# Optimization experiments

Measured on AMD Instinct MI355X. Metric: run time of the kernel, lower is better.

Reference implementation:

```python
import jax, jax.numpy as jnp
import numpy as np

B, T, D = 8, 4096, 768
H, HD, K = 12, 64, 32
TAU, THRESH = 12.5, 0.5
A_PARAM, B_PARAM, DT = 0.7, 0.8, 1.0  # nn.Parameters read via .item() -> scalar constants
N_FHN_STEPS = 2


def setup_inputs() -> dict:
    key = jax.random.key(0)
    k0, k1, k2, k3 = jax.random.split(key, 4)
    x = jax.random.normal(k0, (B, T, D), jnp.float32)
    spectral_basis = jax.random.normal(k1, (B, T, K), jnp.float32)
    w_qkv = jax.random.normal(k2, (3 * D, D), jnp.float32) * 0.02
    w_out = jax.random.normal(k3, (D, D), jnp.float32) * 0.02
    spectral_filter = jnp.ones((H, 32), jnp.float32) * 0.5
    return {"x": x, "spectral_basis": spectral_basis, "w_qkv": w_qkv,
            "w_out": w_out, "spectral_filter": spectral_filter}


def _fhn(stim):
    # Original expands stim [b,h,k] -> [b,h,k,head_dim] (constant along d), runs FHN,
    # then means over d. Values are identical along d, so amax over d == |stim| and the
    # mean is the identity; the math collapses exactly to per-element dynamics on [b,h,k].
    scale = jnp.maximum(jnp.abs(stim), 1e-6)          # == abs().amax(-1).clamp(1e-6)
    stim_normed = stim / scale
    gate = jax.nn.sigmoid((jnp.abs(stim) - THRESH) * 10.0)
    I = stim_normed * (0.1 + 0.9 * gate)
    alpha = DT / TAU
    denom = 1.0 + alpha * B_PARAM
    v = jnp.zeros_like(stim)
    w = jnp.zeros_like(stim)
    for _ in range(N_FHN_STEPS):  # fixed small n_steps, unrolled
        dv = v - (v * v * v) / 3.0 - w + I
        v_next = v + dv * DT
        w_next = (w + (v_next + A_PARAM) * alpha) / denom
        v = jnp.clip(v_next, -3.0, 3.0)
        w = jnp.clip(w_next, -3.0, 3.0)
    return v * scale


def reference(x, spectral_basis, w_qkv, w_out, spectral_filter):
    Bs, Ts, Ds = x.shape
    k = spectral_basis.shape[-1]
    qkv = x @ w_qkv.T                                   # [B,T,3D]
    qkv = qkv.reshape(Bs, Ts, 3, H, HD).transpose(2, 0, 3, 1, 4)  # three,b,h,t,d
    q, kk, v = qkv[0], qkv[1], qkv[2]
    q_spec = jnp.einsum('bhtd,btk->bhkd', q, spectral_basis)
    k_spec = jnp.einsum('bhtd,btk->bhkd', kk, spectral_basis)
    attn_spec = jnp.einsum('bhkd,bhkd->bhk', q_spec, k_spec) / (HD ** 0.5)
    filt = jax.nn.sigmoid(spectral_filter[:, :k])       # [H,k]
    attn_spec = attn_spec * filt[None, :, :]
    fhn_response = _fhn(attn_spec)                      # [B,H,k]
    v_spec = jnp.einsum('bhtd,btk->bhkd', v, spectral_basis)
    out_spec = fhn_response[..., None] * v_spec         # [B,H,k,d]
    out = jnp.einsum('bhkd,btk->bhtd', out_spec, spectral_basis)
    out = out.transpose(0, 2, 1, 3).reshape(Bs, Ts, Ds)  # b t (h d)
    return out @ w_out.T
```

## Files before the change

### kernel.cpp

```cpp
#include <hip/hip_runtime.h>

#define Bc 8
#define Tc 4096
#define Dc 768
#define Hc 12
#define HDc 64
#define Kc 32
#define TD3 2304
#define WQKV_F (TD3 * Dc)
#define WALL_F ((TD3 + Dc) * Dc)
#define SB_F (Bc * Tc * Kc)
#define XS_F (Bc * Kc * Dc)

typedef __attribute__((ext_vector_type(8))) short short8;
typedef __attribute__((ext_vector_type(4))) short short4v;
typedef __attribute__((ext_vector_type(4))) float float4v;

__device__ __forceinline__ float bf2f(unsigned short u) {
    unsigned v = ((unsigned)u) << 16;
    return __builtin_bit_cast(float, v);
}
__device__ __forceinline__ unsigned short f2bf(float f) {
    unsigned u = __builtin_bit_cast(unsigned, f);
    u += 0x7FFFu + ((u >> 16) & 1u);
    return (unsigned short)(u >> 16);
}

__device__ __forceinline__ void split8(const float* p, short8& hi, short8& lo) {
#pragma unroll
    for (int i = 0; i < 8; ++i) {
        unsigned short h = f2bf(p[i]);
        hi[i] = (short)h;
        lo[i] = (short)f2bf(p[i] - bf2f(h));
    }
}
__device__ __forceinline__ void split4(const float4v v, short4v& h, short4v& l) {
#pragma unroll
    for (int q = 0; q < 4; ++q) {
        unsigned short hb = f2bf(v[q]);
        h[q] = (short)hb;
        l[q] = (short)f2bf(v[q] - bf2f(hb));
    }
}

__global__ __launch_bounds__(256) void kconv(const float* __restrict__ wqkv,
                                             const float* __restrict__ wout,
                                             const float* __restrict__ sb,
                                             short* __restrict__ w_hi, short* __restrict__ w_lo,
                                             short* __restrict__ sb_hi, short* __restrict__ sb_lo,
                                             short* __restrict__ sbT_hi, short* __restrict__ sbT_lo) {
    int i = (blockIdx.x * 256 + threadIdx.x) * 4;
    if (i < WALL_F) {
        const float* src = (i < WQKV_F) ? (wqkv + i) : (wout + (i - WQKV_F));
        float4v v = *(const float4v*)src;
        short4v h, l;
        split4(v, h, l);
        *(short4v*)(w_hi + i) = h;
        *(short4v*)(w_lo + i) = l;
    } else {
        int j = i - WALL_F;
        float4v v = *(const float4v*)(sb + j);
        short4v h, l;
        split4(v, h, l);
        *(short4v*)(sb_hi + j) = h;
        *(short4v*)(sb_lo + j) = l;
        int b   = j >> 17;
        int rem = j & (Tc * Kc - 1);
        int t = rem >> 5, k = rem & 31;
        size_t tb = (size_t)b * Kc * Tc;
#pragma unroll
        for (int q = 0; q < 4; ++q) {
            sbT_hi[tb + (size_t)(k + q) * Tc + t] = h[q];
            sbT_lo[tb + (size_t)(k + q) * Tc + t] = l[q];
        }
    }
}

__global__ __launch_bounds__(256) void k1_xspec(const float* __restrict__ x,
                                                const short* __restrict__ sbT_hi,
                                                const short* __restrict__ sbT_lo,
                                                float* __restrict__ pb) {
    int tid  = threadIdx.x;
    int w    = tid >> 6;
    int lane = tid & 63;
    int col  = lane & 15;
    int quad = lane >> 4;

    int bid = blockIdx.x;
    int b  = bid >> 6;
    int dt = (bid >> 4) & 3;
    int tc = bid & 15;
    int d0 = dt * 192;
    size_t bT = (size_t)b * Tc + (size_t)tc * 256;

    float4v acc[2][3];
#pragma unroll
    for (int mi = 0; mi < 2; ++mi)
#pragma unroll
        for (int ni = 0; ni < 3; ++ni) acc[mi][ni] = (float4v){0.f, 0.f, 0.f, 0.f};

#pragma unroll 2
    for (int ks = 0; ks < 8; ++ks) {
        int t8 = tc * 256 + ks * 32 + quad * 8;
        short8 ah[2], al[2];
#pragma unroll
        for (int mi = 0; mi < 2; ++mi) {
            size_t ai = ((size_t)b * Kc + mi * 16 + col) * Tc + t8;
            ah[mi] = *(const short8*)(sbT_hi + ai);
            al[mi] = *(const short8*)(sbT_lo + ai);
        }
#pragma unroll
        for (int ni = 0; ni < 3; ++ni) {
            int nc = d0 + (w * 3 + ni) * 16 + col;
            float bv[8];
#pragma unroll
            for (int j = 0; j < 8; ++j)
                bv[j] = x[(bT + ks * 32 + quad * 8 + j) * Dc + nc];
            short8 bh, bl;
            split8(bv, bh, bl);
#pragma unroll
            for (int mi = 0; mi < 2; ++mi) {
                acc[mi][ni] = __builtin_amdgcn_mfma_f32_16x16x32_bf16(ah[mi], bh, acc[mi][ni], 0, 0, 0);
                acc[mi][ni] = __builtin_amdgcn_mfma_f32_16x16x32_bf16(al[mi], bh, acc[mi][ni], 0, 0, 0);
                acc[mi][ni] = __builtin_amdgcn_mfma_f32_16x16x32_bf16(ah[mi], bl, acc[mi][ni], 0, 0, 0);
            }
        }
    }

    float* pbp = pb + (size_t)tc * XS_F;
#pragma unroll
    for (int mi = 0; mi < 2; ++mi)
#pragma unroll
        for (int ni = 0; ni < 3; ++ni)
#pragma unroll
            for (int r = 0; r < 4; ++r) {
                int kk = mi * 16 + quad * 4 + r;
                int dd = d0 + (w * 3 + ni) * 16 + col;
                pbp[((size_t)(b * Kc + kk)) * Dc + dd] = acc[mi][ni][r];
            }
}

__global__ __launch_bounds__(256) void k1r_reduce(const float* __restrict__ pb,
                                                  short* __restrict__ xs_hi,
                                                  short* __restrict__ xs_lo) {
    int i = (blockIdx.x * 256 + threadIdx.x) * 4;
    float4v s = (float4v){0.f, 0.f, 0.f, 0.f};
#pragma unroll
    for (int p = 0; p < 16; ++p) {
        float4v v = *(const float4v*)(pb + (size_t)p * XS_F + i);
#pragma unroll
        for (int q = 0; q < 4; ++q) s[q] += v[q];
    }
    short4v h, l;
    split4(s, h, l);
    *(short4v*)(xs_hi + i) = h;
    *(short4v*)(xs_lo + i) = l;
}

__global__ __launch_bounds__(256) void k2_qkv(const short* __restrict__ xs_hi,
                                              const short* __restrict__ xs_lo,
                                              const short* __restrict__ w_hi,
                                              const short* __restrict__ w_lo,
                                              float* __restrict__ c1) {
    int lane = threadIdx.x & 63;
    int w    = threadIdx.x >> 6;
    int m    = lane & 15, quad = lane >> 4;
    int mb = blockIdx.x & 7;
    int nb = blockIdx.x >> 3;
    int m0 = mb * 32;
    int n0 = nb * 64 + w * 16;

    const short* a0h = xs_hi + (size_t)(m0 + m) * Dc + quad * 8;
    const short* a0l = xs_lo + (size_t)(m0 + m) * Dc + quad * 8;
    const short* a1h = a0h + (size_t)16 * Dc;
    const short* a1l = a0l + (size_t)16 * Dc;
    const short* bhp = w_hi + (size_t)(n0 + m) * Dc + quad * 8;
    const short* blp = w_lo + (size_t)(n0 + m) * Dc + quad * 8;

    float4v acc0 = (float4v){0.f, 0.f, 0.f, 0.f};
    float4v acc1 = (float4v){0.f, 0.f, 0.f, 0.f};
#pragma unroll 4
    for (int s = 0; s < 24; ++s) {
        short8 bh = *(const short8*)(bhp + s * 32);
        short8 bl = *(const short8*)(blp + s * 32);
        short8 h0 = *(const short8*)(a0h + s * 32);
        short8 l0 = *(const short8*)(a0l + s * 32);
        short8 h1 = *(const short8*)(a1h + s * 32);
        short8 l1 = *(const short8*)(a1l + s * 32);
        acc0 = __builtin_amdgcn_mfma_f32_16x16x32_bf16(h0, bh, acc0, 0, 0, 0);
        acc0 = __builtin_amdgcn_mfma_f32_16x16x32_bf16(l0, bh, acc0, 0, 0, 0);
        acc0 = __builtin_amdgcn_mfma_f32_16x16x32_bf16(h0, bl, acc0, 0, 0, 0);
        acc1 = __builtin_amdgcn_mfma_f32_16x16x32_bf16(h1, bh, acc1, 0, 0, 0);
        acc1 = __builtin_amdgcn_mfma_f32_16x16x32_bf16(l1, bh, acc1, 0, 0, 0);
        acc1 = __builtin_amdgcn_mfma_f32_16x16x32_bf16(h1, bl, acc1, 0, 0, 0);
    }
    float* cp0 = c1 + (size_t)(m0 + quad * 4) * TD3 + n0 + m;
    float* cp1 = cp0 + (size_t)16 * TD3;
#pragma unroll
    for (int r = 0; r < 4; ++r) {
        cp0[(size_t)r * TD3] = acc0[r];
        cp1[(size_t)r * TD3] = acc1[r];
    }
}

__global__ __launch_bounds__(64) void k3_fhn(const float* __restrict__ c1,
                                             const float* __restrict__ sfilt,
                                             short* __restrict__ av_hi,
                                             short* __restrict__ av_lo) {
    int idx = blockIdx.x * 64 + threadIdx.x;
    int kk = idx & 31;
    int bh = idx >> 5;
    int h  = bh % Hc;
    int r  = (bh / Hc) * Kc + kk;

    const float* qp = c1 + (size_t)r * TD3 + h * HDc;
    const float* kp = qp + Dc;
    float s = 0.f;
#pragma unroll
    for (int dd = 0; dd < HDc; ++dd) s = fmaf(qp[dd], kp[dd], s);
    s *= 0.125f;

    float filt = 1.f / (1.f + __expf(-sfilt[h * 32 + kk]));
    s *= filt;

    float as    = fabsf(s);
    float scale = fmaxf(as, 1e-6f);
    float sn    = s / scale;
    float gate  = 1.f / (1.f + __expf(-(as - 0.5f) * 10.f));
    float I     = sn * (0.1f + 0.9f * gate);
    const float alpha = 0.08f;
    const float denom = 1.064f;
    float v = 0.f, w = 0.f;
#pragma unroll
    for (int it = 0; it < 2; ++it) {
        float dv = v - (v * v * v) / 3.f - w + I;
        float vn = v + dv;
        float wn = (w + (vn + 0.7f) * alpha) / denom;
        v = fminf(fmaxf(vn, -3.f), 3.f);
        w = fminf(fmaxf(wn, -3.f), 3.f);
    }
    float fv = v * scale;

    const float* vp = c1 + (size_t)r * TD3 + 2 * Dc + h * HDc;
    short* ohp = av_hi + (size_t)r * Dc + h * HDc;
    short* olp = av_lo + (size_t)r * Dc + h * HDc;
#pragma unroll
    for (int i = 0; i < 16; ++i) {
        float4v vv = *(const float4v*)(vp + i * 4);
#pragma unroll
        for (int q = 0; q < 4; ++q) vv[q] *= fv;
        short4v hv, lv;
        split4(vv, hv, lv);
        *(short4v*)(ohp + i * 4) = hv;
        *(short4v*)(olp + i * 4) = lv;
    }
}

__global__ __launch_bounds__(256) void k4_proj(const short* __restrict__ av_hi,
                                               const short* __restrict__ av_lo,
                                               const short* __restrict__ wo_hi,
                                               const short* __restrict__ wo_lo,
                                               short* __restrict__ pT_hi,
                                               short* __restrict__ pT_lo) {
    int wave = blockIdx.x * 4 + (threadIdx.x >> 6);
    int lane = threadIdx.x & 63;
    int mb = wave & 15;
    int nt = wave >> 4;
    int m0 = mb * 16, n0 = nt * 16;
    int m = lane & 15, quad = lane >> 4;

    const short* ahp = av_hi + (size_t)(m0 + m) * Dc + quad * 8;
    const short* alp = av_lo + (size_t)(m0 + m) * Dc + quad * 8;
    const short* bhp = wo_hi + (size_t)(n0 + m) * Dc + quad * 8;
    const short* blp = wo_lo + (size_t)(n0 + m) * Dc + quad * 8;

    float4v acc = (float4v){0.f, 0.f, 0.f, 0.f};
#pragma unroll 4
    for (int s = 0; s < 24; ++s) {
        short8 ah = *(const short8*)(ahp + s * 32);
        short8 al = *(const short8*)(alp + s * 32);
        short8 bh = *(const short8*)(bhp + s * 32);
        short8 bl = *(const short8*)(blp + s * 32);
        acc = __builtin_amdgcn_mfma_f32_16x16x32_bf16(ah, bh, acc, 0, 0, 0);
        acc = __builtin_amdgcn_mfma_f32_16x16x32_bf16(al, bh, acc, 0, 0, 0);
        acc = __builtin_amdgcn_mfma_f32_16x16x32_bf16(ah, bl, acc, 0, 0, 0);
    }
    short4v hv, lv;
    split4(acc, hv, lv);
    size_t o = (size_t)(n0 + m) * (Bc * Kc) + m0 + quad * 4;
    *(short4v*)(pT_hi + o) = hv;
    *(short4v*)(pT_lo + o) = lv;
}

__global__ __launch_bounds__(256) void k5_out(const short* __restrict__ pT_hi,
                                              const short* __restrict__ pT_lo,
                                              const short* __restrict__ sb_hi,
                                              const short* __restrict__ sb_lo,
                                              float* __restrict__ out) {
    int tid  = threadIdx.x;
    int w    = tid >> 6;
    int lane = tid & 63;
    int col  = lane & 15;
    int quad = lane >> 4;

    int bid = blockIdx.x;
    int b  = bid >> 8;
    int tt = (bid >> 2) & 63;
    int et = bid & 3;
    int t0 = tt * 64 + w * 16;
    int e0 = et * 192;

    size_t ao = ((size_t)b * Tc + t0 + col) * Kc + quad * 8;
    short8 ah = *(const short8*)(sb_hi + ao);
    short8 al = *(const short8*)(sb_lo + ao);

    float4v acc[12];
#pragma unroll
    for (int ni = 0; ni < 12; ++ni) acc[ni] = (float4v){0.f, 0.f, 0.f, 0.f};

#pragma unroll
    for (int ni = 0; ni < 12; ++ni) {
        size_t bo = (size_t)(e0 + ni * 16 + col) * (Bc * Kc) + b * 32 + quad * 8;
        short8 bh = *(const short8*)(pT_hi + bo);
        short8 bl = *(const short8*)(pT_lo + bo);
        acc[ni] = __builtin_amdgcn_mfma_f32_16x16x32_bf16(ah, bh, acc[ni], 0, 0, 0);
        acc[ni] = __builtin_amdgcn_mfma_f32_16x16x32_bf16(al, bh, acc[ni], 0, 0, 0);
        acc[ni] = __builtin_amdgcn_mfma_f32_16x16x32_bf16(ah, bl, acc[ni], 0, 0, 0);
    }

    float* op = out + ((size_t)b * Tc + t0 + quad * 4) * Dc + e0 + col;
#pragma unroll
    for (int ni = 0; ni < 12; ++ni)
#pragma unroll
        for (int r = 0; r < 4; ++r)
            op[(size_t)r * Dc + ni * 16] = acc[ni][r];
}

extern "C" void kernel_launch(void* const* d_in, const int* in_sizes, int n_in,
                              void* d_out, int out_size, void* d_ws, size_t ws_size,
                              hipStream_t stream) {
    const float* x     = (const float*)d_in[0];
    const float* sb    = (const float*)d_in[1];
    const float* wqkv  = (const float*)d_in[2];
    const float* wout  = (const float*)d_in[3];
    const float* sfilt = (const float*)d_in[4];
    float* out = (float*)d_out;

    float* pb    = (float*)d_ws;
    short* w_hi  = (short*)(pb + (size_t)16 * XS_F);
    short* w_lo  = w_hi + (size_t)WALL_F;
    short* xs_hi = w_lo + (size_t)WALL_F;
    short* xs_lo = xs_hi + (size_t)XS_F;
    float* c1    = (float*)(xs_lo + (size_t)XS_F);
    short* av_hi = (short*)(c1 + (size_t)Bc * Kc * TD3);
    short* av_lo = av_hi + (size_t)XS_F;
    short* pT_hi = av_lo + (size_t)XS_F;
    short* pT_lo = pT_hi + (size_t)XS_F;
    short* sb_hi = pT_lo + (size_t)XS_F;
    short* sb_lo = sb_hi + (size_t)SB_F;
    short* sbT_hi = sb_lo + (size_t)SB_F;
    short* sbT_lo = sbT_hi + (size_t)SB_F;

    const short* wo_hi = w_hi + (size_t)WQKV_F;
    const short* wo_lo = w_lo + (size_t)WQKV_F;

    hipLaunchKernelGGL(kconv,      dim3(3328), dim3(256), 0, stream, wqkv, wout, sb,
                       w_hi, w_lo, sb_hi, sb_lo, sbT_hi, sbT_lo);
    hipLaunchKernelGGL(k1_xspec,   dim3(512),  dim3(256), 0, stream, x, sbT_hi, sbT_lo, pb);
    hipLaunchKernelGGL(k1r_reduce, dim3(192),  dim3(256), 0, stream, pb, xs_hi, xs_lo);
    hipLaunchKernelGGL(k2_qkv,     dim3(288),  dim3(256), 0, stream, xs_hi, xs_lo, w_hi, w_lo, c1);
    hipLaunchKernelGGL(k3_fhn,     dim3(48),   dim3(64),  0, stream, c1, sfilt, av_hi, av_lo);
    hipLaunchKernelGGL(k4_proj,    dim3(192),  dim3(256), 0, stream, av_hi, av_lo, wo_hi, wo_lo, pT_hi, pT_lo);
    hipLaunchKernelGGL(k5_out,     dim3(2048), dim3(256), 0, stream, pT_hi, pT_lo, sb_hi, sb_lo, out);
}
```

Before: 284.4 us.

## Transpose spectral basis via shared-memory tile and shrink tiles for more blocks

```diff
diff --git a/kernel.cpp b/kernel.cpp
--- a/kernel.cpp
+++ b/kernel.cpp
@@ -49,30 +49,52 @@
                                              short* __restrict__ w_hi, short* __restrict__ w_lo,
                                              short* __restrict__ sb_hi, short* __restrict__ sb_lo,
                                              short* __restrict__ sbT_hi, short* __restrict__ sbT_lo) {
-    int i = (blockIdx.x * 256 + threadIdx.x) * 4;
-    if (i < WALL_F) {
+    __shared__ float tile[128][33];
+    int bid = blockIdx.x, tid = threadIdx.x;
+
+    if (bid < 2304) {
+        int i = (bid * 256 + tid) * 4;
         const float* src = (i < WQKV_F) ? (wqkv + i) : (wout + (i - WQKV_F));
         float4v v = *(const float4v*)src;
         short4v h, l;
         split4(v, h, l);
         *(short4v*)(w_hi + i) = h;
         *(short4v*)(w_lo + i) = l;
-    } else {
-        int j = i - WALL_F;
-        float4v v = *(const float4v*)(sb + j);
+        return;
+    }
+
+    int sbi = bid - 2304;
+    int b  = sbi >> 5;
+    int tt = sbi & 31;
+    size_t base = ((size_t)b * Tc + tt * 128) * Kc;
+
+#pragma unroll
+    for (int p = 0; p < 4; ++p) {
+        int f4  = tid + p * 256;
+        int row = f4 >> 3, c4 = f4 & 7;
+        size_t o = base + (size_t)row * Kc + c4 * 4;
+        float4v v = *(const float4v*)(sb + o);
         short4v h, l;
         split4(v, h, l);
-        *(short4v*)(sb_hi + j) = h;
-        *(short4v*)(sb_lo + j) = l;
-        int b   = j >> 17;
-        int rem = j & (Tc * Kc - 1);
-        int t = rem >> 5, k = rem & 31;
-        size_t tb = (size_t)b * Kc * Tc;
-#pragma unroll
-        for (int q = 0; q < 4; ++q) {
-            sbT_hi[tb + (size_t)(k + q) * Tc + t] = h[q];
-            sbT_lo[tb + (size_t)(k + q) * Tc + t] = l[q];
-        }
+        *(short4v*)(sb_hi + o) = h;
+        *(short4v*)(sb_lo + o) = l;
+#pragma unroll
+        for (int q = 0; q < 4; ++q) tile[row][c4 * 4 + q] = v[q];
+    }
+    __syncthreads();
+
+    size_t tb = (size_t)b * Kc * Tc + tt * 128;
+#pragma unroll
+    for (int p = 0; p < 2; ++p) {
+        int u  = tid + p * 256;
+        int k  = u >> 4, ts = u & 15;
+        float av[8];
+#pragma unroll
+        for (int j = 0; j < 8; ++j) av[j] = tile[ts * 8 + j][k];
+        short8 h, l;
+        split8(av, h, l);
+        *(short8*)(sbT_hi + tb + (size_t)k * Tc + ts * 8) = h;
+        *(short8*)(sbT_lo + tb + (size_t)k * Tc + ts * 8) = l;
     }
 }
 
@@ -87,17 +109,16 @@
     int quad = lane >> 4;
 
     int bid = blockIdx.x;
-    int b  = bid >> 6;
-    int dt = (bid >> 4) & 3;
-    int tc = bid & 15;
-    int d0 = dt * 192;
+    int b  = bid / 192;
+    int r2 = bid % 192;
+    int tc = r2 / 12;
+    int dt = r2 % 12;
+    int nc = dt * 64 + w * 16 + col;
     size_t bT = (size_t)b * Tc + (size_t)tc * 256;
 
-    float4v acc[2][3];
-#pragma unroll
-    for (int mi = 0; mi < 2; ++mi)
-#pragma unroll
-        for (int ni = 0; ni < 3; ++ni) acc[mi][ni] = (float4v){0.f, 0.f, 0.f, 0.f};
+    float4v acc[2];
+    acc[0] = (float4v){0.f, 0.f, 0.f, 0.f};
+    acc[1] = (float4v){0.f, 0.f, 0.f, 0.f};
 
 #pragma unroll 2
     for (int ks = 0; ks < 8; ++ks) {
@@ -109,21 +130,17 @@
             ah[mi] = *(const short8*)(sbT_hi + ai);
             al[mi] = *(const short8*)(sbT_lo + ai);
         }
-#pragma unroll
-        for (int ni = 0; ni < 3; ++ni) {
-            int nc = d0 + (w * 3 + ni) * 16 + col;
-            float bv[8];
-#pragma unroll
-            for (int j = 0; j < 8; ++j)
-                bv[j] = x[(bT + ks * 32 + quad * 8 + j) * Dc + nc];
-            short8 bh, bl;
-            split8(bv, bh, bl);
-#pragma unroll
-            for (int mi = 0; mi < 2; ++mi) {
-                acc[mi][ni] = __builtin_amdgcn_mfma_f32_16x16x32_bf16(ah[mi], bh, acc[mi][ni], 0, 0, 0);
-                acc[mi][ni] = __builtin_amdgcn_mfma_f32_16x16x32_bf16(al[mi], bh, acc[mi][ni], 0, 0, 0);
-                acc[mi][ni] = __builtin_amdgcn_mfma_f32_16x16x32_bf16(ah[mi], bl, acc[mi][ni], 0, 0, 0);
-            }
+        float bv[8];
+#pragma unroll
+        for (int j = 0; j < 8; ++j)
+            bv[j] = x[(bT + ks * 32 + quad * 8 + j) * Dc + nc];
+        short8 bh, bl;
+        split8(bv, bh, bl);
+#pragma unroll
+        for (int mi = 0; mi < 2; ++mi) {
+            acc[mi] = __builtin_amdgcn_mfma_f32_16x16x32_bf16(ah[mi], bh, acc[mi], 0, 0, 0);
+            acc[mi] = __builtin_amdgcn_mfma_f32_16x16x32_bf16(al[mi], bh, acc[mi], 0, 0, 0);
+            acc[mi] = __builtin_amdgcn_mfma_f32_16x16x32_bf16(ah[mi], bl, acc[mi], 0, 0, 0);
         }
     }
 
@@ -131,13 +148,10 @@
 #pragma unroll
     for (int mi = 0; mi < 2; ++mi)
 #pragma unroll
-        for (int ni = 0; ni < 3; ++ni)
-#pragma unroll
-            for (int r = 0; r < 4; ++r) {
-                int kk = mi * 16 + quad * 4 + r;
-                int dd = d0 + (w * 3 + ni) * 16 + col;
-                pbp[((size_t)(b * Kc + kk)) * Dc + dd] = acc[mi][ni][r];
-            }
+        for (int r = 0; r < 4; ++r) {
+            int kk = mi * 16 + quad * 4 + r;
+            pbp[((size_t)(b * Kc + kk)) * Dc + nc] = acc[mi][r];
+        }
 }
 
 __global__ __launch_bounds__(256) void k1r_reduce(const float* __restrict__ pb,
@@ -165,42 +179,30 @@
     int lane = threadIdx.x & 63;
     int w    = threadIdx.x >> 6;
     int m    = lane & 15, quad = lane >> 4;
-    int mb = blockIdx.x & 7;
-    int nb = blockIdx.x >> 3;
-    int m0 = mb * 32;
+    int mb = blockIdx.x & 15;
+    int nb = blockIdx.x >> 4;
+    int m0 = mb * 16;
     int n0 = nb * 64 + w * 16;
 
-    const short* a0h = xs_hi + (size_t)(m0 + m) * Dc + quad * 8;
-    const short* a0l = xs_lo + (size_t)(m0 + m) * Dc + quad * 8;
-    const short* a1h = a0h + (size_t)16 * Dc;
-    const short* a1l = a0l + (size_t)16 * Dc;
+    const short* ahp = xs_hi + (size_t)(m0 + m) * Dc + quad * 8;
+    const short* alp = xs_lo + (size_t)(m0 + m) * Dc + quad * 8;
     const short* bhp = w_hi + (size_t)(n0 + m) * Dc + quad * 8;
     const short* blp = w_lo + (size_t)(n0 + m) * Dc + quad * 8;
 
-    float4v acc0 = (float4v){0.f, 0.f, 0.f, 0.f};
-    float4v acc1 = (float4v){0.f, 0.f, 0.f, 0.f};
+    float4v acc = (float4v){0.f, 0.f, 0.f, 0.f};
 #pragma unroll 4
     for (int s = 0; s < 24; ++s) {
+        short8 ah = *(const short8*)(ahp + s * 32);
+        short8 al = *(const short8*)(alp + s * 32);
         short8 bh = *(const short8*)(bhp + s * 32);
         short8 bl = *(const short8*)(blp + s * 32);
-        short8 h0 = *(const short8*)(a0h + s * 32);
-        short8 l0 = *(const short8*)(a0l + s * 32);
-        short8 h1 = *(const short8*)(a1h + s * 32);
-        short8 l1 = *(const short8*)(a1l + s * 32);
-        acc0 = __builtin_amdgcn_mfma_f32_16x16x32_bf16(h0, bh, acc0, 0, 0, 0);
-        acc0 = __builtin_amdgcn_mfma_f32_16x16x32_bf16(l0, bh, acc0, 0, 0, 0);
-        acc0 = __builtin_amdgcn_mfma_f32_16x16x32_bf16(h0, bl, acc0, 0, 0, 0);
-        acc1 = __builtin_amdgcn_mfma_f32_16x16x32_bf16(h1, bh, acc1, 0, 0, 0);
-        acc1 = __builtin_amdgcn_mfma_f32_16x16x32_bf16(l1, bh, acc1, 0, 0, 0);
-        acc1 = __builtin_amdgcn_mfma_f32_16x16x32_bf16(h1, bl, acc1, 0, 0, 0);
-    }
-    float* cp0 = c1 + (size_t)(m0 + quad * 4) * TD3 + n0 + m;
-    float* cp1 = cp0 + (size_t)16 * TD3;
-#pragma unroll
-    for (int r = 0; r < 4; ++r) {
-        cp0[(size_t)r * TD3] = acc0[r];
-        cp1[(size_t)r * TD3] = acc1[r];
-    }
+        acc = __builtin_amdgcn_mfma_f32_16x16x32_bf16(ah, bh, acc, 0, 0, 0);
+        acc = __builtin_amdgcn_mfma_f32_16x16x32_bf16(al, bh, acc, 0, 0, 0);
+        acc = __builtin_amdgcn_mfma_f32_16x16x32_bf16(ah, bl, acc, 0, 0, 0);
+    }
+    float* cp = c1 + (size_t)(m0 + quad * 4) * TD3 + n0 + m;
+#pragma unroll
+    for (int r = 0; r < 4; ++r) cp[(size_t)r * TD3] = acc[r];
 }
 
 __global__ __launch_bounds__(64) void k3_fhn(const float* __restrict__ c1,
@@ -364,11 +366,11 @@
     const short* wo_hi = w_hi + (size_t)WQKV_F;
     const short* wo_lo = w_lo + (size_t)WQKV_F;
 
-    hipLaunchKernelGGL(kconv,      dim3(3328), dim3(256), 0, stream, wqkv, wout, sb,
+    hipLaunchKernelGGL(kconv,      dim3(2560), dim3(256), 0, stream, wqkv, wout, sb,
                        w_hi, w_lo, sb_hi, sb_lo, sbT_hi, sbT_lo);
-    hipLaunchKernelGGL(k1_xspec,   dim3(512),  dim3(256), 0, stream, x, sbT_hi, sbT_lo, pb);
+    hipLaunchKernelGGL(k1_xspec,   dim3(1536), dim3(256), 0, stream, x, sbT_hi, sbT_lo, pb);
     hipLaunchKernelGGL(k1r_reduce, dim3(192),  dim3(256), 0, stream, pb, xs_hi, xs_lo);
-    hipLaunchKernelGGL(k2_qkv,     dim3(288),  dim3(256), 0, stream, xs_hi, xs_lo, w_hi, w_lo, c1);
+    hipLaunchKernelGGL(k2_qkv,     dim3(576),  dim3(256), 0, stream, xs_hi, xs_lo, w_hi, w_lo, c1);
     hipLaunchKernelGGL(k3_fhn,     dim3(48),   dim3(64),  0, stream, c1, sfilt, av_hi, av_lo);
     hipLaunchKernelGGL(k4_proj,    dim3(192),  dim3(256), 0, stream, av_hi, av_lo, wo_hi, wo_lo, pT_hi, pT_lo);
     hipLaunchKernelGGL(k5_out,     dim3(2048), dim3(256), 0, stream, pT_hi, pT_lo, sb_hi, sb_lo, out);
```

New measurement: 290.8 us. +2.3%, slower.
